# Optimization experiments

Hardware: AMD Instinct MI355X
Metric: run time of the kernel (lower is better)

## Reference

```python
import jax, jax.numpy as jnp
import numpy as np

B, S, D, H = 4, 2048, 1024, 16
HD = D // H  # 64


def setup_inputs() -> dict:
    key = jax.random.key(0)
    k1, k2, k3, k4, k5 = jax.random.split(key, 5)
    scale = 0.02
    return {
        "hidden_states": jax.random.normal(k1, (B, S, D), dtype=jnp.float32),
        "c_attn_w": jax.random.normal(k2, (D, 3 * D), dtype=jnp.float32) * scale,
        "c_attn_b": jax.random.normal(k3, (3 * D,), dtype=jnp.float32) * scale,
        "c_proj_w": jax.random.normal(k4, (D, D), dtype=jnp.float32) * scale,
        "c_proj_b": jax.random.normal(k5, (D,), dtype=jnp.float32) * scale,
    }


def reference(hidden_states, c_attn_w, c_attn_b, c_proj_w, c_proj_b):
    b, s, d = hidden_states.shape
    # Conv1D: x @ W + b, fused QKV
    qkv = hidden_states @ c_attn_w + c_attn_b  # [b, s, 3d]
    q, k, v = jnp.split(qkv, 3, axis=-1)
    # split heads -> [b, h, s, hd]
    def split_heads(x):
        return x.reshape(b, s, H, HD).transpose(0, 2, 1, 3)
    q, k, v = split_heads(q), split_heads(k), split_heads(v)
    # scaled dot-product attention with causal mask (eager GPT-2 math)
    scores = jnp.einsum("bhqd,bhkd->bhqk", q, k) / jnp.asarray(HD ** 0.5, q.dtype)
    causal = jnp.tril(jnp.ones((s, s), dtype=bool))  # [s, s]
    mask_value = jnp.asarray(jnp.finfo(scores.dtype).min, scores.dtype)
    scores = jnp.where(causal[None, None, :, :], scores, mask_value)
    attn = jax.nn.softmax(scores, axis=-1)
    out = jnp.einsum("bhqk,bhkd->bhqd", attn, v)  # [b, h, s, hd]
    out = out.transpose(0, 2, 1, 3).reshape(b, s, d)  # merge heads
    out = out @ c_proj_w + c_proj_b
    return out
```

## Files before the change

kernel.cpp:

```cpp
#include <hip/hip_runtime.h>
#include <hip/hip_bf16.h>
#include <stdint.h>

#define B_ 4
#define S_ 2048
#define D_ 1024
#define H_ 16
#define HD_ 64

typedef __bf16 bf16_t;
typedef bf16_t bf16x8 __attribute__((ext_vector_type(8)));
typedef bf16_t bf16x4 __attribute__((ext_vector_type(4)));
typedef float f32x4 __attribute__((ext_vector_type(4)));
typedef float f32x16 __attribute__((ext_vector_type(16)));

__device__ __forceinline__ bf16x8 cvt8(f32x4 lo, f32x4 hi) {
  bf16x8 r;
#pragma unroll
  for (int i = 0; i < 4; i++) {
    r[i] = (bf16_t)lo[i];
    r[i + 4] = (bf16_t)hi[i];
  }
  return r;
}

__device__ __forceinline__ void async_lds16(const bf16_t* g, bf16_t* l) {
  __builtin_amdgcn_global_load_lds(
      (const __attribute__((address_space(1))) void*)g,
      (__attribute__((address_space(3))) void*)l, 16, 0, 0);
}

__device__ __forceinline__ uint32_t pk2(float a, float b) {
  union {
    bf16_t h[2];
    uint32_t u;
  } x;
  x.h[0] = (bf16_t)a;
  x.h[1] = (bf16_t)b;
  return x.u;
}

__device__ __forceinline__ void swap32(uint32_t& a, uint32_t& b) {
  asm("v_permlane32_swap_b32 %0, %1" : "+v"(a), "+v"(b));
}

union PAU {
  uint32_t w[4];
  bf16x8 v;
};

__global__ __launch_bounds__(256) void cvt_f32_bf16(
    const float* __restrict__ in, bf16_t* __restrict__ out) {
  size_t i = ((size_t)blockIdx.x * 256 + threadIdx.x) * 8;
  f32x4 lo = *(const f32x4*)(in + i);
  f32x4 hi = *(const f32x4*)(in + i + 4);
  *(bf16x8*)(out + i) = cvt8(lo, hi);
}

__global__ void transpose_cvt(const float* __restrict__ in,
                              bf16_t* __restrict__ out, int R, int C) {
  __shared__ bf16_t tile[32][33];
  int c0 = blockIdx.x * 32, r0 = blockIdx.y * 32;
  int tx = threadIdx.x, ty = threadIdx.y;
  for (int i = ty; i < 32; i += 8)
    tile[i][tx] = (bf16_t)in[(size_t)(r0 + i) * C + c0 + tx];
  __syncthreads();
  for (int i = ty; i < 32; i += 8)
    out[(size_t)(c0 + i) * R + r0 + tx] = tile[tx][i];
}

__global__ __launch_bounds__(256) void gemm_bt(
    const void* __restrict__ A, const bf16_t* __restrict__ BT,
    const float* __restrict__ bias, float* __restrict__ Cout,
    bf16_t* __restrict__ qws, bf16_t* __restrict__ kws,
    bf16_t* __restrict__ vws, int M, int Nw, int K, int mode, int a_is_f32,
    size_t a_off) {
  __shared__ bf16_t As[128 * 32];
  __shared__ bf16_t Bs[128 * 32];
  const int tid = threadIdx.x;
  const int wave = tid >> 6, lane = tid & 63;
  const int quad = lane >> 4, tn = lane & 15;
  const int lid = blockIdx.y * gridDim.x + blockIdx.x;
  const int cpx = (gridDim.x * gridDim.y) >> 3;
  const int nl = (lid & 7) * cpx + (lid >> 3);
  const int m_blk = (nl / gridDim.x) * 128, n_blk = (nl % gridDim.x) * 128;
  const int wm = (wave >> 1) * 64, wn = (wave & 1) * 64;

  f32x4 acc[4][4] = {};

  const int srow = wave * 32 + (lane >> 2);
  const int scol = (lane & 3) * 8;
  size_t aoff = a_off + (size_t)(m_blk + srow) * K + scol;
  const bf16_t* gb = BT + (size_t)(n_blk + srow) * K + scol;
  bf16_t* lbB0 = &Bs[wave * 1024];
  bf16_t* lbB1 = &Bs[wave * 1024 + 512];
  bf16_t* laA0 = &As[wave * 1024];
  bf16_t* laA1 = &As[wave * 1024 + 512];

  for (int k0 = 0; k0 < K; k0 += 32) {
    async_lds16(gb, lbB0);
    async_lds16(gb + (size_t)16 * K, lbB1);
    if (a_is_f32) {
      const float* gaf = (const float*)A + aoff;
      f32x4 a00 = *(const f32x4*)gaf;
      f32x4 a01 = *(const f32x4*)(gaf + 4);
      f32x4 a10 = *(const f32x4*)(gaf + (size_t)16 * K);
      f32x4 a11 = *(const f32x4*)(gaf + (size_t)16 * K + 4);
      *(bf16x8*)&As[srow * 32 + scol] = cvt8(a00, a01);
      *(bf16x8*)&As[(srow + 16) * 32 + scol] = cvt8(a10, a11);
    } else {
      const bf16_t* ga = (const bf16_t*)A + aoff;
      async_lds16(ga, laA0);
      async_lds16(ga + (size_t)16 * K, laA1);
    }
    aoff += 32;
    gb += 32;
    __syncthreads();

    bf16x8 af[4], bfr[4];
#pragma unroll
    for (int i = 0; i < 4; i++)
      af[i] = *(const bf16x8*)&As[(wm + i * 16 + tn) * 32 + quad * 8];
#pragma unroll
    for (int i = 0; i < 4; i++)
      bfr[i] = *(const bf16x8*)&Bs[(wn + i * 16 + tn) * 32 + quad * 8];
#pragma unroll
    for (int mi = 0; mi < 4; mi++)
#pragma unroll
      for (int ni = 0; ni < 4; ni++)
        acc[mi][ni] = __builtin_amdgcn_mfma_f32_16x16x32_bf16(af[mi], bfr[ni],
                                                              acc[mi][ni], 0, 0, 0);
    __syncthreads();
  }

  if (mode == 0) {
#pragma unroll
    for (int ni = 0; ni < 4; ni++) {
      int n = n_blk + wn + ni * 16 + tn;
      float bv = bias[n];
#pragma unroll
      for (int mi = 0; mi < 4; mi++)
#pragma unroll
        for (int r = 0; r < 4; r++) {
          int m = m_blk + wm + mi * 16 + quad * 4 + r;
          Cout[(size_t)m * Nw + n] = acc[mi][ni][r] + bv;
        }
    }
  } else {
#pragma unroll
    for (int ni = 0; ni < 4; ni++) {
      int n = n_blk + wn + ni * 16 + tn;
      int sec = n >> 10;
      int hn = n & 1023;
      int hh = hn >> 6, hd = hn & 63;
      float bv = bias[n];
      if (sec == 2) {
#pragma unroll
        for (int mi = 0; mi < 4; mi++) {
          int m = m_blk + wm + mi * 16 + quad * 4;
          int bb = m >> 11, s = m & 2047;
          bf16x4 pk;
#pragma unroll
          for (int r = 0; r < 4; r++) pk[r] = (bf16_t)(acc[mi][ni][r] + bv);
          *(bf16x4*)&vws[((size_t)(bb * H_ + hh) * HD_ + hd) * S_ + s] = pk;
        }
      } else {
        bf16_t* dst = (sec == 0) ? qws : kws;
#pragma unroll
        for (int mi = 0; mi < 4; mi++)
#pragma unroll
          for (int r = 0; r < 4; r++) {
            int m = m_blk + wm + mi * 16 + quad * 4 + r;
            int bb = m >> 11, s = m & 2047;
            dst[((size_t)(bb * H_ + hh) * S_ + s) * HD_ + hd] =
                (bf16_t)(acc[mi][ni][r] + bv);
          }
      }
    }
  }
}

__global__ __launch_bounds__(512, 2) void attn_kernel(
    const bf16_t* __restrict__ Qw, const bf16_t* __restrict__ Kw,
    const bf16_t* __restrict__ VTw, bf16_t* __restrict__ Ow) {
  __shared__ bf16_t Ks[2][64 * 64];
  __shared__ bf16_t Vt[2][64 * 64];

  const int tid = threadIdx.x;
  const int wave = tid >> 6, lane = tid & 63;
  const int lq = lane & 31;
  const int h = lane >> 5;
  const int qoff = h * 4;
  const int bid = blockIdx.x;
  const int j = bid >> 3;
  const int bh = (bid & 7) * 8 + (j >> 2);
  const int pj = j & 3;

  const bf16_t* Qb = Qw + (size_t)bh * S_ * HD_;
  const bf16_t* Kb = Kw + (size_t)bh * S_ * HD_;
  const bf16_t* VTb = VTw + (size_t)bh * HD_ * S_;

  const float kScale = 0.125f * 1.44269504088896f;

  bf16x8 onesf;
#pragma unroll
  for (int jj = 0; jj < 8; jj++) onesf[jj] = (bf16_t)1.0f;

  const float NEG = -30000.0f;
  const int b = bh >> 4, hh = bh & 15;

  const int srow = wave * 8 + (lane >> 3);
  const int sslot = lane & 7;
  const bf16_t* kp = Kb + (size_t)srow * HD_ + (sslot ^ (srow & 7)) * 8;
  const bf16_t* vp = VTb + (size_t)srow * S_ + (sslot ^ (srow & 7)) * 8;

#define STAGE(buf, kt)                                                 \
  do {                                                                 \
    async_lds16(kp + (size_t)(kt) * (64 * HD_), &Ks[buf][wave * 512]); \
    async_lds16(vp + (size_t)(kt) * 64, &Vt[buf][wave * 512]);         \
  } while (0)

  for (int task = 0; task < 2; task++) {
    const int qt = task == 0 ? (7 - pj) : pj;
    const int qb = qt * 256;
    const int qa = qb + ((lq >> 3) << 6) + wave * 8 + (lq & 7);

    bf16x8 qf[4];
#pragma unroll
    for (int kg = 0; kg < 4; kg++) {
      bf16x8 v = *(const bf16x8*)&Qb[(size_t)qa * HD_ + kg * 16 + h * 8];
#pragma unroll
      for (int jj = 0; jj < 8; jj++) v[jj] = (bf16_t)((float)v[jj] * kScale);
      qf[kg] = v;
    }

    f32x16 o0 = {}, o1 = {};
    f32x16 ls = {};
    float mrow = NEG;

    const int kt_max = (qb + 255) >> 6;

    if (task) __syncthreads();
    STAGE(0, 0);

    for (int kt = 0; kt <= kt_max; kt++) {
      __syncthreads();
      if (kt < kt_max) STAGE((kt + 1) & 1, kt + 1);

      const bf16_t* KsB = Ks[kt & 1];
      const bf16_t* VtB = Vt[kt & 1];
      const int rsl = lq & 7;

      f32x16 st0 = {}, st1 = {};
      __builtin_amdgcn_s_setprio(1);
#pragma unroll
      for (int kg = 0; kg < 4; kg++) {
        const int slot = kg * 2 + h;
        bf16x8 kf0 = *(const bf16x8*)&KsB[lq * 64 + ((slot ^ rsl) * 8)];
        bf16x8 kf1 = *(const bf16x8*)&KsB[(32 + lq) * 64 + ((slot ^ rsl) * 8)];
        st0 = __builtin_amdgcn_mfma_f32_32x32x16_bf16(kf0, qf[kg], st0, 0, 0, 0);
        st1 = __builtin_amdgcn_mfma_f32_32x32x16_bf16(kf1, qf[kg], st1, 0, 0, 0);
      }
      __builtin_amdgcn_s_setprio(0);
      if (kt * 64 + 63 > qb) {
#pragma unroll
        for (int r = 0; r < 16; r++) {
          int key0 = kt * 64 + (r & 3) + 8 * (r >> 2) + qoff;
          if (key0 > qa) st0[r] = NEG;
          if (key0 + 32 > qa) st1[r] = NEG;
        }
      }
      float m8[8];
#pragma unroll
      for (int i = 0; i < 4; i++) {
        m8[i] = fmaxf(fmaxf(st0[4 * i], st0[4 * i + 1]),
                      fmaxf(st0[4 * i + 2], st0[4 * i + 3]));
        m8[4 + i] = fmaxf(fmaxf(st1[4 * i], st1[4 * i + 1]),
                          fmaxf(st1[4 * i + 2], st1[4 * i + 3]));
      }
      float mx = fmaxf(fmaxf(fmaxf(m8[0], m8[1]), fmaxf(m8[2], m8[3])),
                       fmaxf(fmaxf(m8[4], m8[5]), fmaxf(m8[6], m8[7])));
      mx = fmaxf(mx, __shfl_xor(mx, 32, 64));

      if (__any(mx > mrow + 8.f)) {
        float mnew = fmaxf(mrow, mx);
        float alpha = exp2f(mrow - mnew);
        mrow = mnew;
#pragma unroll
        for (int r = 0; r < 16; r++) {
          float ar = __shfl(alpha, (r & 3) + 8 * (r >> 2) + qoff, 64);
          o0[r] *= ar;
          o1[r] *= ar;
          ls[r] *= ar;
        }
      }
#pragma unroll
      for (int r = 0; r < 16; r++) {
        st0[r] = exp2f(st0[r] - mrow);
        st1[r] = exp2f(st1[r] - mrow);
      }

      PAU pa[4];
      {
        uint32_t w[8];
#pragma unroll
        for (int i = 0; i < 8; i++) w[i] = pk2(st0[2 * i], st0[2 * i + 1]);
        swap32(w[0], w[2]);
        swap32(w[1], w[3]);
        swap32(w[4], w[6]);
        swap32(w[5], w[7]);
        pa[0].w[0] = w[0]; pa[0].w[1] = w[1]; pa[0].w[2] = w[2]; pa[0].w[3] = w[3];
        pa[1].w[0] = w[4]; pa[1].w[1] = w[5]; pa[1].w[2] = w[6]; pa[1].w[3] = w[7];
#pragma unroll
        for (int i = 0; i < 8; i++) w[i] = pk2(st1[2 * i], st1[2 * i + 1]);
        swap32(w[0], w[2]);
        swap32(w[1], w[3]);
        swap32(w[4], w[6]);
        swap32(w[5], w[7]);
        pa[2].w[0] = w[0]; pa[2].w[1] = w[1]; pa[2].w[2] = w[2]; pa[2].w[3] = w[3];
        pa[3].w[0] = w[4]; pa[3].w[1] = w[5]; pa[3].w[2] = w[6]; pa[3].w[3] = w[7];
      }

      __builtin_amdgcn_s_setprio(1);
#pragma unroll
      for (int kg = 0; kg < 4; kg++) {
        const int slot = kg * 2 + h;
        bf16x8 vf0 = *(const bf16x8*)&VtB[lq * 64 + ((slot ^ rsl) * 8)];
        bf16x8 vf1 = *(const bf16x8*)&VtB[(32 + lq) * 64 + ((slot ^ rsl) * 8)];
        o0 = __builtin_amdgcn_mfma_f32_32x32x16_bf16(pa[kg].v, vf0, o0, 0, 0, 0);
        o1 = __builtin_amdgcn_mfma_f32_32x32x16_bf16(pa[kg].v, vf1, o1, 0, 0, 0);
        ls = __builtin_amdgcn_mfma_f32_32x32x16_bf16(pa[kg].v, onesf, ls, 0, 0, 0);
      }
      __builtin_amdgcn_s_setprio(0);
    }

#pragma unroll
    for (int r = 0; r < 16; r++) {
      int qr = (r & 3) + 8 * (r >> 2) + qoff;
      int q = qb + ((qr >> 3) << 6) + wave * 8 + (qr & 7);
      float inv = 1.f / fmaxf(ls[r], 1e-30f);
      bf16_t* dst = Ow + (size_t)(b * S_ + q) * D_ + hh * HD_;
      dst[lq] = (bf16_t)(o0[r] * inv);
      dst[32 + lq] = (bf16_t)(o1[r] * inv);
    }
  }
#undef STAGE
}

extern "C" void kernel_launch(void* const* d_in, const int* in_sizes, int n_in,
                              void* d_out, int out_size, void* d_ws,
                              size_t ws_size, hipStream_t stream) {
  const float* hidden = nullptr;
  const float* attn_w = nullptr;
  const float* attn_b = nullptr;
  const float* proj_w = nullptr;
  const float* proj_b = nullptr;
  for (int i = 0; i < n_in; ++i) {
    switch (in_sizes[i]) {
      case 8388608: hidden = (const float*)d_in[i]; break;
      case 3145728: attn_w = (const float*)d_in[i]; break;
      case 3072:    attn_b = (const float*)d_in[i]; break;
      case 1048576: proj_w = (const float*)d_in[i]; break;
      case 1024:    proj_b = (const float*)d_in[i]; break;
      default: break;
    }
  }
  if (!hidden) hidden = (const float*)d_in[0];
  if (!attn_w) attn_w = (const float*)d_in[1];
  if (!attn_b) attn_b = (const float*)d_in[2];
  if (!proj_w) proj_w = (const float*)d_in[3];
  if (!proj_b) proj_b = (const float*)d_in[4];
  float* out = (float*)d_out;

  char* ws = (char*)d_ws;
  const size_t AWS_B = (size_t)B_ * S_ * D_ * 2;
  const size_t QKV_E = (size_t)B_ * H_ * S_ * HD_;

  bf16_t* aws = (bf16_t*)ws;
  bf16_t* wT1 = (bf16_t*)ws;
  bf16_t* qws = (bf16_t*)(ws + AWS_B);
  bf16_t* kws = qws + QKV_E;
  bf16_t* vws = kws + QKV_E;
  bf16_t* wT2 = qws;
  bf16_t* hb = (bf16_t*)d_out;

  cvt_f32_bf16<<<dim3(4096), 256, 0, stream>>>(hidden, hb);
  transpose_cvt<<<dim3(96, 32), dim3(32, 8), 0, stream>>>(attn_w, wT1, 1024, 3072);
  gemm_bt<<<dim3(24, 64), 256, 0, stream>>>(
      hb, wT1, attn_b, nullptr, qws, kws, vws, 8192, 3072, 1024, 1, 0, 0);
  attn_kernel<<<dim3(256), 512, 0, stream>>>(qws, kws, vws, aws);
  transpose_cvt<<<dim3(32, 32), dim3(32, 8), 0, stream>>>(proj_w, wT2, 1024, 1024);
  gemm_bt<<<dim3(8, 64), 256, 0, stream>>>(
      aws, wT2, proj_b, out, nullptr, nullptr, nullptr, 8192, 1024, 1024, 0, 0, 0);
}
```

Measured before the change: 285.7 us.

## Process 128-key tiles per attention iteration and fuse input prep kernels

The attention kernel now stages and processes 128 keys per loop iteration instead of 64. K and V tiles are loaded with four async copies per stage, scores sit in four 32x32 accumulators, and the P·V loop runs over eight k-groups. This halves the number of barriers, softmax max-reductions and rescale checks per query tile. The hidden-state conversion and the QKV weight transpose are merged into one launch to save a kernel launch. In exchange, LDS use doubles and register pressure rises under the 512x2 launch bound, which risks spills or lower occupancy.

```diff
diff --git a/kernel.cpp b/kernel.cpp
--- a/kernel.cpp
+++ b/kernel.cpp
@@ -49,12 +49,27 @@
   bf16x8 v;
 };
 
-__global__ __launch_bounds__(256) void cvt_f32_bf16(
-    const float* __restrict__ in, bf16_t* __restrict__ out) {
-  size_t i = ((size_t)blockIdx.x * 256 + threadIdx.x) * 8;
-  f32x4 lo = *(const f32x4*)(in + i);
-  f32x4 hi = *(const f32x4*)(in + i + 4);
-  *(bf16x8*)(out + i) = cvt8(lo, hi);
+__global__ __launch_bounds__(256) void prep(
+    const float* __restrict__ hidden, bf16_t* __restrict__ hb,
+    const float* __restrict__ attn_w, bf16_t* __restrict__ wT1) {
+  __shared__ bf16_t tile[32][33];
+  const int bid = blockIdx.x;
+  if (bid < 4096) {
+    size_t i = ((size_t)bid * 256 + threadIdx.x) * 8;
+    f32x4 lo = *(const f32x4*)(hidden + i);
+    f32x4 hi = *(const f32x4*)(hidden + i + 4);
+    *(bf16x8*)(hb + i) = cvt8(lo, hi);
+  } else {
+    const int b2 = bid - 4096;
+    const int c0 = (b2 % 96) * 32, r0 = (b2 / 96) * 32;
+    const int tx = threadIdx.x & 31, ty = threadIdx.x >> 5;
+    const int R = 1024, C = 3072;
+    for (int i = ty; i < 32; i += 8)
+      tile[i][tx] = (bf16_t)attn_w[(size_t)(r0 + i) * C + c0 + tx];
+    __syncthreads();
+    for (int i = ty; i < 32; i += 8)
+      wT1[(size_t)(c0 + i) * R + r0 + tx] = tile[tx][i];
+  }
 }
 
 __global__ void transpose_cvt(const float* __restrict__ in,
@@ -183,8 +198,8 @@
 __global__ __launch_bounds__(512, 2) void attn_kernel(
     const bf16_t* __restrict__ Qw, const bf16_t* __restrict__ Kw,
     const bf16_t* __restrict__ VTw, bf16_t* __restrict__ Ow) {
-  __shared__ bf16_t Ks[2][64 * 64];
-  __shared__ bf16_t Vt[2][64 * 64];
+  __shared__ bf16_t Ks[2][128 * 64];
+  __shared__ bf16_t Vt[2][64 * 128];
 
   const int tid = threadIdx.x;
   const int wave = tid >> 6, lane = tid & 63;
@@ -209,15 +224,24 @@
   const float NEG = -30000.0f;
   const int b = bh >> 4, hh = bh & 15;
 
-  const int srow = wave * 8 + (lane >> 3);
-  const int sslot = lane & 7;
-  const bf16_t* kp = Kb + (size_t)srow * HD_ + (sslot ^ (srow & 7)) * 8;
-  const bf16_t* vp = VTb + (size_t)srow * S_ + (sslot ^ (srow & 7)) * 8;
-
-#define STAGE(buf, kt)                                                 \
-  do {                                                                 \
-    async_lds16(kp + (size_t)(kt) * (64 * HD_), &Ks[buf][wave * 512]); \
-    async_lds16(vp + (size_t)(kt) * 64, &Vt[buf][wave * 512]);         \
+  const int krow = wave * 16 + (lane >> 3);
+  const int ksl = lane & 7;
+  const bf16_t* kpA = Kb + (size_t)krow * HD_ + ((ksl ^ (krow & 7)) * 8);
+  const bf16_t* kpB =
+      Kb + (size_t)(krow + 8) * HD_ + ((ksl ^ ((krow + 8) & 7)) * 8);
+  const int vrow = wave * 8 + (lane >> 4);
+  const int vsl = lane & 15;
+  const bf16_t* vpA = VTb + (size_t)vrow * S_ + ((vsl ^ (vrow & 7)) * 8);
+  const bf16_t* vpB =
+      VTb + (size_t)(vrow + 4) * S_ + ((vsl ^ ((vrow + 4) & 7)) * 8);
+
+#define STAGE(buf, kt)                                                     \
+  do {                                                                     \
+    async_lds16(kpA + (size_t)(kt) * (128 * HD_), &Ks[buf][wave * 1024]);  \
+    async_lds16(kpB + (size_t)(kt) * (128 * HD_),                          \
+                &Ks[buf][wave * 1024 + 512]);                              \
+    async_lds16(vpA + (size_t)(kt) * 128, &Vt[buf][wave * 1024]);          \
+    async_lds16(vpB + (size_t)(kt) * 128, &Vt[buf][wave * 1024 + 512]);    \
   } while (0)
 
   for (int task = 0; task < 2; task++) {
@@ -238,7 +262,7 @@
     f32x16 ls = {};
     float mrow = NEG;
 
-    const int kt_max = (qb + 255) >> 6;
+    const int kt_max = (qb + 255) >> 7;
 
     if (task) __syncthreads();
     STAGE(0, 0);
@@ -251,36 +275,47 @@
       const bf16_t* VtB = Vt[kt & 1];
       const int rsl = lq & 7;
 
-      f32x16 st0 = {}, st1 = {};
+      f32x16 st[4] = {{}, {}, {}, {}};
       __builtin_amdgcn_s_setprio(1);
 #pragma unroll
       for (int kg = 0; kg < 4; kg++) {
         const int slot = kg * 2 + h;
-        bf16x8 kf0 = *(const bf16x8*)&KsB[lq * 64 + ((slot ^ rsl) * 8)];
-        bf16x8 kf1 = *(const bf16x8*)&KsB[(32 + lq) * 64 + ((slot ^ rsl) * 8)];
-        st0 = __builtin_amdgcn_mfma_f32_32x32x16_bf16(kf0, qf[kg], st0, 0, 0, 0);
-        st1 = __builtin_amdgcn_mfma_f32_32x32x16_bf16(kf1, qf[kg], st1, 0, 0, 0);
+#pragma unroll
+        for (int bk = 0; bk < 4; bk++) {
+          bf16x8 kf = *(const bf16x8*)&KsB[(bk * 32 + lq) * 64 +
+                                           ((slot ^ rsl) * 8)];
+          st[bk] =
+              __builtin_amdgcn_mfma_f32_32x32x16_bf16(kf, qf[kg], st[bk], 0, 0, 0);
+        }
       }
       __builtin_amdgcn_s_setprio(0);
-      if (kt * 64 + 63 > qb) {
-#pragma unroll
-        for (int r = 0; r < 16; r++) {
-          int key0 = kt * 64 + (r & 3) + 8 * (r >> 2) + qoff;
-          if (key0 > qa) st0[r] = NEG;
-          if (key0 + 32 > qa) st1[r] = NEG;
+      if (kt * 128 + 127 > qb) {
+#pragma unroll
+        for (int bk = 0; bk < 4; bk++)
+#pragma unroll
+          for (int r = 0; r < 16; r++) {
+            int key = kt * 128 + bk * 32 + (r & 3) + 8 * (r >> 2) + qoff;
+            if (key > qa) st[bk][r] = NEG;
+          }
+      }
+      float mx;
+      {
+        float m4[4];
+#pragma unroll
+        for (int bk = 0; bk < 4; bk++) {
+          float a0 = fmaxf(fmaxf(st[bk][0], st[bk][1]),
+                           fmaxf(st[bk][2], st[bk][3]));
+          float a1 = fmaxf(fmaxf(st[bk][4], st[bk][5]),
+                           fmaxf(st[bk][6], st[bk][7]));
+          float a2 = fmaxf(fmaxf(st[bk][8], st[bk][9]),
+                           fmaxf(st[bk][10], st[bk][11]));
+          float a3 = fmaxf(fmaxf(st[bk][12], st[bk][13]),
+                           fmaxf(st[bk][14], st[bk][15]));
+          m4[bk] = fmaxf(fmaxf(a0, a1), fmaxf(a2, a3));
         }
-      }
-      float m8[8];
-#pragma unroll
-      for (int i = 0; i < 4; i++) {
-        m8[i] = fmaxf(fmaxf(st0[4 * i], st0[4 * i + 1]),
-                      fmaxf(st0[4 * i + 2], st0[4 * i + 3]));
-        m8[4 + i] = fmaxf(fmaxf(st1[4 * i], st1[4 * i + 1]),
-                          fmaxf(st1[4 * i + 2], st1[4 * i + 3]));
-      }
-      float mx = fmaxf(fmaxf(fmaxf(m8[0], m8[1]), fmaxf(m8[2], m8[3])),
-                       fmaxf(fmaxf(m8[4], m8[5]), fmaxf(m8[6], m8[7])));
-      mx = fmaxf(mx, __shfl_xor(mx, 32, 64));
+        mx = fmaxf(fmaxf(m4[0], m4[1]), fmaxf(m4[2], m4[3]));
+        mx = fmaxf(mx, __shfl_xor(mx, 32, 64));
+      }
 
       if (__any(mx > mrow + 8.f)) {
         float mnew = fmaxf(mrow, mx);
@@ -295,38 +330,38 @@
         }
       }
 #pragma unroll
-      for (int r = 0; r < 16; r++) {
-        st0[r] = exp2f(st0[r] - mrow);
-        st1[r] = exp2f(st1[r] - mrow);
-      }
-
-      PAU pa[4];
-      {
+      for (int bk = 0; bk < 4; bk++)
+#pragma unroll
+        for (int r = 0; r < 16; r++) st[bk][r] = exp2f(st[bk][r] - mrow);
+
+      PAU pa[8];
+#pragma unroll
+      for (int bk = 0; bk < 4; bk++) {
         uint32_t w[8];
 #pragma unroll
-        for (int i = 0; i < 8; i++) w[i] = pk2(st0[2 * i], st0[2 * i + 1]);
+        for (int i = 0; i < 8; i++)
+          w[i] = pk2(st[bk][2 * i], st[bk][2 * i + 1]);
         swap32(w[0], w[2]);
         swap32(w[1], w[3]);
         swap32(w[4], w[6]);
         swap32(w[5], w[7]);
-        pa[0].w[0] = w[0]; pa[0].w[1] = w[1]; pa[0].w[2] = w[2]; pa[0].w[3] = w[3];
-        pa[1].w[0] = w[4]; pa[1].w[1] = w[5]; pa[1].w[2] = w[6]; pa[1].w[3] = w[7];
-#pragma unroll
-        for (int i = 0; i < 8; i++) w[i] = pk2(st1[2 * i], st1[2 * i + 1]);
-        swap32(w[0], w[2]);
-        swap32(w[1], w[3]);
-        swap32(w[4], w[6]);
-        swap32(w[5], w[7]);
-        pa[2].w[0] = w[0]; pa[2].w[1] = w[1]; pa[2].w[2] = w[2]; pa[2].w[3] = w[3];
-        pa[3].w[0] = w[4]; pa[3].w[1] = w[5]; pa[3].w[2] = w[6]; pa[3].w[3] = w[7];
+        pa[2 * bk].w[0] = w[0];
+        pa[2 * bk].w[1] = w[1];
+        pa[2 * bk].w[2] = w[2];
+        pa[2 * bk].w[3] = w[3];
+        pa[2 * bk + 1].w[0] = w[4];
+        pa[2 * bk + 1].w[1] = w[5];
+        pa[2 * bk + 1].w[2] = w[6];
+        pa[2 * bk + 1].w[3] = w[7];
       }
 
       __builtin_amdgcn_s_setprio(1);
 #pragma unroll
-      for (int kg = 0; kg < 4; kg++) {
+      for (int kg = 0; kg < 8; kg++) {
         const int slot = kg * 2 + h;
-        bf16x8 vf0 = *(const bf16x8*)&VtB[lq * 64 + ((slot ^ rsl) * 8)];
-        bf16x8 vf1 = *(const bf16x8*)&VtB[(32 + lq) * 64 + ((slot ^ rsl) * 8)];
+        bf16x8 vf0 = *(const bf16x8*)&VtB[lq * 128 + ((slot ^ rsl) * 8)];
+        bf16x8 vf1 =
+            *(const bf16x8*)&VtB[(32 + lq) * 128 + ((slot ^ rsl) * 8)];
         o0 = __builtin_amdgcn_mfma_f32_32x32x16_bf16(pa[kg].v, vf0, o0, 0, 0, 0);
         o1 = __builtin_amdgcn_mfma_f32_32x32x16_bf16(pa[kg].v, vf1, o1, 0, 0, 0);
         ls = __builtin_amdgcn_mfma_f32_32x32x16_bf16(pa[kg].v, onesf, ls, 0, 0, 0);
@@ -384,8 +419,7 @@
   bf16_t* wT2 = qws;
   bf16_t* hb = (bf16_t*)d_out;
 
-  cvt_f32_bf16<<<dim3(4096), 256, 0, stream>>>(hidden, hb);
-  transpose_cvt<<<dim3(96, 32), dim3(32, 8), 0, stream>>>(attn_w, wT1, 1024, 3072);
+  prep<<<dim3(7168), 256, 0, stream>>>(hidden, hb, attn_w, wT1);
   gemm_bt<<<dim3(24, 64), 256, 0, stream>>>(
       hb, wT1, attn_b, nullptr, qws, kws, vws, 8192, 3072, 1024, 1, 0, 0);
   attn_kernel<<<dim3(256), 512, 0, stream>>>(qws, kws, vws, aws);
```

Measured after the change: 287.2 us. Within noise of the previous version (+0.5%).
